# Performance work log

Hardware: AMD Instinct MI355X
Metric: run time of the kernel (lower is better)

Reference implementation:

```python
import jax, jax.numpy as jnp
import numpy as np

PAA_SIZE = 64  # init_kwargs paa_size
GAF_TYPE = 'GADF'  # init_kwargs GAF_type


def setup_inputs() -> dict:
    key = jax.random.key(0)
    x = jax.random.uniform(key, (256, 4096, 32), dtype=jnp.float32)
    return {"x": x}


def reference(x):
    # x: [B, T, C]
    B, T, C = x.shape
    # --- rescale: per-sample, per-channel min-max over time axis -> [0, 1]
    x_min = jnp.min(x, axis=1, keepdims=True)
    x_max = jnp.max(x, axis=1, keepdims=True)
    r = (x - x_min) / (x_max - x_min)            # [B, T, C]
    # --- PAA: strided mean over bins of length size = T // paa_size
    size = T // PAA_SIZE
    p = r[:, : PAA_SIZE * size].reshape(B, PAA_SIZE, size, C).sum(axis=2) / size  # [B, P, C]
    # --- GAF construction
    y = jnp.sqrt(1.0 - p * p)                    # [B, P, C]
    if GAF_TYPE == 'GASF':
        # out[b,i,j,c] = x_i x_j - y_i y_j (symmetric)
        out = jnp.einsum('bic,bjc->bijc', p, p) - jnp.einsum('bic,bjc->bijc', y, y)
    else:  # 'GADF'
        # original: -transpose(y x^T - x y^T) => out[b,i,j,c] = y_i x_j - x_i y_j
        out = jnp.einsum('bic,bjc->bijc', y, p) - jnp.einsum('bic,bjc->bijc', p, y)
    return out  # [B, paa_size, paa_size, C]
```

## Files before the change

kernel.cpp:

```cpp
#include <hip/hip_runtime.h>
#include <math.h>

#define BB   256
#define TT   4096
#define CC   32
#define PP   64
#define PSTR 36

__device__ __forceinline__ float4 f4min(float4 a, float4 b) {
    return make_float4(fminf(a.x,b.x), fminf(a.y,b.y), fminf(a.z,b.z), fminf(a.w,b.w));
}
__device__ __forceinline__ float4 f4max(float4 a, float4 b) {
    return make_float4(fmaxf(a.x,b.x), fmaxf(a.y,b.y), fmaxf(a.z,b.z), fmaxf(a.w,b.w));
}
__device__ __forceinline__ void f4add(float4& a, float4 v) {
    a.x += v.x; a.y += v.y; a.z += v.z; a.w += v.w;
}
__device__ __forceinline__ float4 shflxor4(float4 v, int m) {
    return make_float4(__shfl_xor(v.x, m), __shfl_xor(v.y, m),
                       __shfl_xor(v.z, m), __shfl_xor(v.w, m));
}

__global__ __launch_bounds__(1024) void gaf_kernel(const float* __restrict__ x,
                                                   float* __restrict__ out) {
    __shared__ float sp[PP * PSTR];
    __shared__ float sy[PP * PSTR];
    __shared__ float redmin[16 * CC];
    __shared__ float redmax[16 * CC];

    const int tid  = threadIdx.x;
    const int cg   = tid & 7;
    const int rb   = tid >> 3;
    const int wave = tid >> 6;
    const int lane = tid & 63;
    const int b    = blockIdx.x;

    const float4* x4 = (const float4*)x + (size_t)b * (TT * CC / 4) + rb * 256 + cg;

    const float FBIG = 3.402823466e+38f;
    float4 mn = make_float4(FBIG, FBIG, FBIG, FBIG);
    float4 mx = make_float4(-FBIG, -FBIG, -FBIG, -FBIG);
    float4 acc = make_float4(0.f, 0.f, 0.f, 0.f);

    #pragma unroll 8
    for (int k = 0; k < 32; ++k) {
        float4 v = x4[k * 8];
        mn = f4min(mn, v); mx = f4max(mx, v); f4add(acc, v);
    }

    float4 seg = acc;
    f4add(seg, shflxor4(acc, 8));

    #pragma unroll
    for (int m = 8; m <= 32; m <<= 1) {
        mn = f4min(mn, shflxor4(mn, m));
        mx = f4max(mx, shflxor4(mx, m));
    }
    if (lane < 8) {
        *(float4*)&redmin[wave * CC + cg * 4] = mn;
        *(float4*)&redmax[wave * CC + cg * 4] = mx;
    }
    __syncthreads();

    float4 gmn = *(const float4*)&redmin[0 * CC + cg * 4];
    float4 gmx = *(const float4*)&redmax[0 * CC + cg * 4];
    #pragma unroll
    for (int w = 1; w < 16; ++w) {
        gmn = f4min(gmn, *(const float4*)&redmin[w * CC + cg * 4]);
        gmx = f4max(gmx, *(const float4*)&redmax[w * CC + cg * 4]);
    }

    if ((rb & 1) == 0) {
        const int s = rb >> 1;
        float4 inv;
        inv.x = 1.0f / (gmx.x - gmn.x);
        inv.y = 1.0f / (gmx.y - gmn.y);
        inv.z = 1.0f / (gmx.z - gmn.z);
        inv.w = 1.0f / (gmx.w - gmn.w);
        const float s64 = 1.0f / 64.0f;
        float4 p, y;
        p.x = (seg.x * s64 - gmn.x) * inv.x;  p.y = (seg.y * s64 - gmn.y) * inv.y;
        p.z = (seg.z * s64 - gmn.z) * inv.z;  p.w = (seg.w * s64 - gmn.w) * inv.w;
        y.x = sqrtf(fmaxf(1.f - p.x * p.x, 0.f));  y.y = sqrtf(fmaxf(1.f - p.y * p.y, 0.f));
        y.z = sqrtf(fmaxf(1.f - p.z * p.z, 0.f));  y.w = sqrtf(fmaxf(1.f - p.w * p.w, 0.f));
        *(float4*)&sp[s * PSTR + cg * 4] = p;
        *(float4*)&sy[s * PSTR + cg * 4] = y;
    }
    __syncthreads();

    const int j  = (tid >> 3) & 63;
    const int ih = tid >> 9;
    const float4 pj = *(const float4*)&sp[j * PSTR + cg * 4];
    const float4 yj = *(const float4*)&sy[j * PSTR + cg * 4];

    float4* o4 = (float4*)out + (size_t)b * (PP * PP * CC / 4);

    #pragma unroll 8
    for (int ii = 0; ii < 32; ++ii) {
        const int i = ih * 32 + ii;
        const float4 pi = *(const float4*)&sp[i * PSTR + cg * 4];
        const float4 yi = *(const float4*)&sy[i * PSTR + cg * 4];
        float4 r;
        r.x = yi.x * pj.x - pi.x * yj.x;  r.y = yi.y * pj.y - pi.y * yj.y;
        r.z = yi.z * pj.z - pi.z * yj.z;  r.w = yi.w * pj.w - pi.w * yj.w;
        o4[i * 512 + j * 8 + cg] = r;
    }
}

extern "C" void kernel_launch(void* const* d_in, const int* in_sizes, int n_in,
                              void* d_out, int out_size, void* d_ws, size_t ws_size,
                              hipStream_t stream) {
    const float* x = (const float*)d_in[0];
    float* out = (float*)d_out;
    gaf_kernel<<<BB, 1024, 0, stream>>>(x, out);
}
```

Before: 237.8 us.

## Give each wave contiguous time segments with batched loads and contiguous output rows

Each wave now reads a contiguous 256-row time chunk, covering four PAA segments. It issues eight float4 loads at a time before reducing, and keeps four segment sums reduced with shuffles instead of a pairwise partial sum. In the output stage each wave writes four full contiguous i-rows, reusing register-cached j values, instead of striding across i. The aim is more memory requests in flight and fully contiguous per-wave read and write streams. The LDS row stride changes to 33, which makes the float4 LDS accesses misaligned, and the launch-bounds occupancy hint adds register pressure.

```diff
diff --git a/kernel.cpp b/kernel.cpp
--- a/kernel.cpp
+++ b/kernel.cpp
@@ -5,7 +5,7 @@
 #define TT   4096
 #define CC   32
 #define PP   64
-#define PSTR 36
+#define PSTR 33
 
 __device__ __forceinline__ float4 f4min(float4 a, float4 b) {
     return make_float4(fminf(a.x,b.x), fminf(a.y,b.y), fminf(a.z,b.z), fminf(a.w,b.w));
@@ -21,41 +21,47 @@
                        __shfl_xor(v.z, m), __shfl_xor(v.w, m));
 }
 
-__global__ __launch_bounds__(1024) void gaf_kernel(const float* __restrict__ x,
-                                                   float* __restrict__ out) {
+__global__ __launch_bounds__(1024, 4) void gaf_kernel(const float* __restrict__ x,
+                                                      float* __restrict__ out) {
     __shared__ float sp[PP * PSTR];
     __shared__ float sy[PP * PSTR];
     __shared__ float redmin[16 * CC];
     __shared__ float redmax[16 * CC];
 
     const int tid  = threadIdx.x;
-    const int cg   = tid & 7;
-    const int rb   = tid >> 3;
+    const int lane = tid & 63;
     const int wave = tid >> 6;
-    const int lane = tid & 63;
+    const int cg   = lane & 7;
     const int b    = blockIdx.x;
 
-    const float4* x4 = (const float4*)x + (size_t)b * (TT * CC / 4) + rb * 256 + cg;
+    const float4* xw = (const float4*)x + (size_t)b * (TT * CC / 4) + wave * 2048 + lane;
 
     const float FBIG = 3.402823466e+38f;
     float4 mn = make_float4(FBIG, FBIG, FBIG, FBIG);
     float4 mx = make_float4(-FBIG, -FBIG, -FBIG, -FBIG);
-    float4 acc = make_float4(0.f, 0.f, 0.f, 0.f);
+    float4 acc[4];
+    #pragma unroll
+    for (int g = 0; g < 4; ++g) acc[g] = make_float4(0.f, 0.f, 0.f, 0.f);
 
-    #pragma unroll 8
-    for (int k = 0; k < 32; ++k) {
-        float4 v = x4[k * 8];
-        mn = f4min(mn, v); mx = f4max(mx, v); f4add(acc, v);
+    #pragma unroll
+    for (int g = 0; g < 4; ++g) {
+        float4 buf[8];
+        #pragma unroll
+        for (int u = 0; u < 8; ++u) buf[u] = xw[(g * 8 + u) * 64];
+        #pragma unroll
+        for (int u = 0; u < 8; ++u) {
+            mn = f4min(mn, buf[u]); mx = f4max(mx, buf[u]); f4add(acc[g], buf[u]);
+        }
     }
-
-    float4 seg = acc;
-    f4add(seg, shflxor4(acc, 8));
 
     #pragma unroll
     for (int m = 8; m <= 32; m <<= 1) {
         mn = f4min(mn, shflxor4(mn, m));
         mx = f4max(mx, shflxor4(mx, m));
+        #pragma unroll
+        for (int g = 0; g < 4; ++g) f4add(acc[g], shflxor4(acc[g], m));
     }
+
     if (lane < 8) {
         *(float4*)&redmin[wave * CC + cg * 4] = mn;
         *(float4*)&redmax[wave * CC + cg * 4] = mx;
@@ -70,40 +76,51 @@
         gmx = f4max(gmx, *(const float4*)&redmax[w * CC + cg * 4]);
     }
 
-    if ((rb & 1) == 0) {
-        const int s = rb >> 1;
-        float4 inv;
-        inv.x = 1.0f / (gmx.x - gmn.x);
-        inv.y = 1.0f / (gmx.y - gmn.y);
-        inv.z = 1.0f / (gmx.z - gmn.z);
-        inv.w = 1.0f / (gmx.w - gmn.w);
-        const float s64 = 1.0f / 64.0f;
-        float4 p, y;
-        p.x = (seg.x * s64 - gmn.x) * inv.x;  p.y = (seg.y * s64 - gmn.y) * inv.y;
-        p.z = (seg.z * s64 - gmn.z) * inv.z;  p.w = (seg.w * s64 - gmn.w) * inv.w;
-        y.x = sqrtf(fmaxf(1.f - p.x * p.x, 0.f));  y.y = sqrtf(fmaxf(1.f - p.y * p.y, 0.f));
-        y.z = sqrtf(fmaxf(1.f - p.z * p.z, 0.f));  y.w = sqrtf(fmaxf(1.f - p.w * p.w, 0.f));
-        *(float4*)&sp[s * PSTR + cg * 4] = p;
-        *(float4*)&sy[s * PSTR + cg * 4] = y;
+    float4 inv;
+    inv.x = 1.0f / (gmx.x - gmn.x);  inv.y = 1.0f / (gmx.y - gmn.y);
+    inv.z = 1.0f / (gmx.z - gmn.z);  inv.w = 1.0f / (gmx.w - gmn.w);
+    const float s64 = 1.0f / 64.0f;
+
+    if (lane < 8) {
+        #pragma unroll
+        for (int g = 0; g < 4; ++g) {
+            float4 p, y;
+            p.x = (acc[g].x * s64 - gmn.x) * inv.x;  p.y = (acc[g].y * s64 - gmn.y) * inv.y;
+            p.z = (acc[g].z * s64 - gmn.z) * inv.z;  p.w = (acc[g].w * s64 - gmn.w) * inv.w;
+            y.x = sqrtf(fmaxf(1.f - p.x * p.x, 0.f));  y.y = sqrtf(fmaxf(1.f - p.y * p.y, 0.f));
+            y.z = sqrtf(fmaxf(1.f - p.z * p.z, 0.f));  y.w = sqrtf(fmaxf(1.f - p.w * p.w, 0.f));
+            const int s = wave * 4 + g;
+            *(float4*)&sp[s * PSTR + cg * 4] = p;
+            *(float4*)&sy[s * PSTR + cg * 4] = y;
+        }
     }
     __syncthreads();
 
-    const int j  = (tid >> 3) & 63;
-    const int ih = tid >> 9;
-    const float4 pj = *(const float4*)&sp[j * PSTR + cg * 4];
-    const float4 yj = *(const float4*)&sy[j * PSTR + cg * 4];
+    const int jrow = lane >> 3;
+    float4 pj[8], yj[8];
+    #pragma unroll
+    for (int jc = 0; jc < 8; ++jc) {
+        const int j = jc * 8 + jrow;
+        pj[jc] = *(const float4*)&sp[j * PSTR + cg * 4];
+        yj[jc] = *(const float4*)&sy[j * PSTR + cg * 4];
+    }
 
-    float4* o4 = (float4*)out + (size_t)b * (PP * PP * CC / 4);
+    float4* ob = (float4*)out + (size_t)b * (PP * PP * CC / 4) + wave * 2048 + lane;
 
-    #pragma unroll 8
-    for (int ii = 0; ii < 32; ++ii) {
-        const int i = ih * 32 + ii;
+    #pragma unroll
+    for (int ii = 0; ii < 4; ++ii) {
+        const int i = wave * 4 + ii;
         const float4 pi = *(const float4*)&sp[i * PSTR + cg * 4];
         const float4 yi = *(const float4*)&sy[i * PSTR + cg * 4];
-        float4 r;
-        r.x = yi.x * pj.x - pi.x * yj.x;  r.y = yi.y * pj.y - pi.y * yj.y;
-        r.z = yi.z * pj.z - pi.z * yj.z;  r.w = yi.w * pj.w - pi.w * yj.w;
-        o4[i * 512 + j * 8 + cg] = r;
+        #pragma unroll
+        for (int jc = 0; jc < 8; ++jc) {
+            float4 r;
+            r.x = yi.x * pj[jc].x - pi.x * yj[jc].x;
+            r.y = yi.y * pj[jc].y - pi.y * yj[jc].y;
+            r.z = yi.z * pj[jc].z - pi.z * yj[jc].z;
+            r.w = yi.w * pj[jc].w - pi.w * yj[jc].w;
+            ob[ii * 512 + jc * 64] = r;
+        }
     }
 }
 
```

After: 231.3 us. 2.7% less time.
